# Performance work log

Hardware: AMD Instinct MI355X
Metric: run time of the kernel (lower is better)

## Reference

```python
import jax, jax.numpy as jnp
import numpy as np

BINS = 10

def setup_inputs() -> dict:
    key = jax.random.key(0)
    k1, k2 = jax.random.split(key)
    N, C = 262144, 512
    x = jax.random.normal(k1, (N, C), dtype=jnp.float32)
    target = jax.random.randint(k2, (N,), 0, C, dtype=jnp.int64)
    return {"x": x, "target": target}

def reference(x, target):
    # log-softmax + NLL (reduction='none', no class weights)
    log_p = jax.nn.log_softmax(x, axis=-1)                      # [N, C]
    log_pt = jnp.take_along_axis(log_p, target[:, None].astype(jnp.int32), axis=1)[:, 0]  # [N]
    ce = -log_pt                                                # NLL per-sample
    # gradient-norm proxy g = |pt - 1|, detached
    g = jax.lax.stop_gradient(jnp.abs(jnp.exp(log_pt) - 1.0))   # [N]
    bin_idx = jnp.floor(g * (BINS - 0.0001)).astype(jnp.int32)  # [N] in [0, BINS)
    # histogram (first call: _last_bin_count is None -> raw counts, no EMA)
    bin_count = jnp.zeros((BINS,), dtype=x.dtype).at[bin_idx].add(1.0)
    nonempty = jnp.sum(bin_count > 0).astype(x.dtype)
    gd = jnp.maximum(bin_count * nonempty, 0.0001)
    beta = 1.0 / gd                                             # [BINS]
    loss = jax.lax.stop_gradient(beta[bin_idx]) * ce            # [N]
    return loss.mean()                                          # reduction='mean'
```

## Files before the change

### kernel.cpp

```cpp
#include <hip/hip_runtime.h>
#include <hip/hip_bf16.h>

#define BINS 10
#define C 512

__global__ __launch_bounds__(256) void ghmc_pass1(const float* __restrict__ x,
                                                  const int* __restrict__ target,
                                                  float* __restrict__ gbins,
                                                  int N) {
    __shared__ float s_cnt[BINS];
    __shared__ float s_sum[BINS];
    const int tid = threadIdx.x;
    if (tid < BINS) { s_cnt[tid] = 0.0f; s_sum[tid] = 0.0f; }
    __syncthreads();

    const int sub = tid & 15;
    const int grp = tid >> 4;
    const int row0   = blockIdx.x * 16 + grp;
    const int stride = gridDim.x * 16;

    for (int row = row0; row < N; row += stride) {
        const float* rowp = x + (size_t)row * C;
        const float4* rp4 = (const float4*)rowp;

        float4 v[8];
        #pragma unroll
        for (int j = 0; j < 8; ++j) v[j] = rp4[sub + 16 * j];

        float s = 0.0f;
        #pragma unroll
        for (int j = 0; j < 8; ++j)
            s += __expf(v[j].x) + __expf(v[j].y) + __expf(v[j].z) + __expf(v[j].w);

        #pragma unroll
        for (int off = 8; off >= 1; off >>= 1)
            s += __shfl_xor(s, off);

        float lse = __logf(s);

        int   tgt = target[row];
        float xt  = rowp[tgt];
        float ce  = lse - xt;
        float pt  = __expf(xt - lse);
        float g   = fabsf(pt - 1.0f);
        int   bin = (int)(g * (BINS - 0.0001f));
        bin = bin < 0 ? 0 : (bin > BINS - 1 ? BINS - 1 : bin);

        if (sub == 0) {
            atomicAdd(&s_cnt[bin], 1.0f);
            atomicAdd(&s_sum[bin], ce);
        }
    }

    __syncthreads();
    if (tid < BINS) {
        atomicAdd(&gbins[tid],        s_cnt[tid]);
        atomicAdd(&gbins[BINS + tid], s_sum[tid]);
    }
}

__global__ void ghmc_pass2(const float* __restrict__ gbins,
                           float* __restrict__ out, float invN) {
    if (threadIdx.x == 0 && blockIdx.x == 0) {
        int ne = 0;
        #pragma unroll
        for (int b = 0; b < BINS; ++b)
            if (gbins[b] > 0.0f) ne++;
        float nef = (float)ne;
        float acc = 0.0f;
        #pragma unroll
        for (int b = 0; b < BINS; ++b) {
            float gd = fmaxf(gbins[b] * nef, 0.0001f);
            acc += gbins[BINS + b] / gd;
        }
        out[0] = acc * invN;
    }
}

extern "C" void kernel_launch(void* const* d_in, const int* in_sizes, int n_in,
                              void* d_out, int out_size, void* d_ws, size_t ws_size,
                              hipStream_t stream) {
    const float* x      = (const float*)d_in[0];
    const int*   target = (const int*)d_in[1];
    float*       out    = (float*)d_out;
    float*       gbins  = (float*)d_ws;

    const int N = in_sizes[1];

    hipMemsetAsync(gbins, 0, 2 * BINS * sizeof(float), stream);

    ghmc_pass1<<<2048, 256, 0, stream>>>(x, target, gbins, N);
    ghmc_pass2<<<1, 64, 0, stream>>>(gbins, out, 1.0f / (float)N);
}
```

Measured before the change: 121.9 us.

## Fuse finalize into main kernel via last-block counter and double-row prefetch

Merges the second single-thread finalize kernel into the main kernel using a global atomic ticket counter, so the last block to finish computes the final loss. It also processes two rows per loop iteration, issuing both rows' loads before computing to raise memory-level parallelism. This removes one kernel launch and its gap, at the cost of higher register pressure and a serialized tail in the last block.

```diff
diff --git a/kernel.cpp b/kernel.cpp
--- a/kernel.cpp
+++ b/kernel.cpp
@@ -4,91 +4,123 @@
 #define BINS 10
 #define C 512
 
-__global__ __launch_bounds__(256) void ghmc_pass1(const float* __restrict__ x,
+
+__device__ __forceinline__ void process_row(const float* __restrict__ rowp,
+                                            const float4 (&v)[8],
+                                            int sub, int tgt,
+                                            float* s_cnt, float* s_sum) {
+    float xt = rowp[tgt];
+    float s = 0.0f;
+    #pragma unroll
+    for (int j = 0; j < 8; ++j)
+        s += __expf(v[j].x) + __expf(v[j].y) + __expf(v[j].z) + __expf(v[j].w);
+    #pragma unroll
+    for (int off = 8; off >= 1; off >>= 1)
+        s += __shfl_xor(s, off);
+    float lse = __logf(s);
+    float ce  = lse - xt;
+    float pt  = __expf(xt - lse);
+    float g   = fabsf(pt - 1.0f);
+    int   bin = (int)(g * (BINS - 0.0001f));
+    bin = bin < 0 ? 0 : (bin > BINS - 1 ? BINS - 1 : bin);
+    if (sub == 0) {
+        atomicAdd(&s_cnt[bin], 1.0f);
+        atomicAdd(&s_sum[bin], ce);
+    }
+}
+
+__global__ __launch_bounds__(256) void ghmc_fused(const float* __restrict__ x,
                                                   const int* __restrict__ target,
                                                   float* __restrict__ gbins,
-                                                  int N) {
+                                                  unsigned int* __restrict__ counter,
+                                                  float* __restrict__ out,
+                                                  int N, float invN) {
     __shared__ float s_cnt[BINS];
     __shared__ float s_sum[BINS];
     const int tid = threadIdx.x;
     if (tid < BINS) { s_cnt[tid] = 0.0f; s_sum[tid] = 0.0f; }
     __syncthreads();
 
-    const int sub = tid & 15;
-    const int grp = tid >> 4;
+    const int sub    = tid & 15;
+    const int grp    = tid >> 4;
+    const int stride = gridDim.x * 16;
     const int row0   = blockIdx.x * 16 + grp;
-    const int stride = gridDim.x * 16;
 
-    for (int row = row0; row < N; row += stride) {
-        const float* rowp = x + (size_t)row * C;
-        const float4* rp4 = (const float4*)rowp;
+    for (int row = row0; row < N; row += 2 * stride) {
+        const int rowB = row + stride;
+        const bool hasB = rowB < N;
 
-        float4 v[8];
+        const float* rowpA = x + (size_t)row * C;
+        const float4* rpA  = (const float4*)rowpA;
+        int tgtA = target[row];
+        float4 a[8];
         #pragma unroll
-        for (int j = 0; j < 8; ++j) v[j] = rp4[sub + 16 * j];
+        for (int j = 0; j < 8; ++j) a[j] = rpA[sub + 16 * j];
 
-        float s = 0.0f;
-        #pragma unroll
-        for (int j = 0; j < 8; ++j)
-            s += __expf(v[j].x) + __expf(v[j].y) + __expf(v[j].z) + __expf(v[j].w);
+        const float* rowpB = x + (size_t)rowB * C;
+        const float4* rpB  = (const float4*)rowpB;
+        int tgtB = 0;
+        float4 b[8];
+        if (hasB) {
+            tgtB = target[rowB];
+            #pragma unroll
+            for (int j = 0; j < 8; ++j) b[j] = rpB[sub + 16 * j];
+        }
 
-        #pragma unroll
-        for (int off = 8; off >= 1; off >>= 1)
-            s += __shfl_xor(s, off);
-
-        float lse = __logf(s);
-
-        int   tgt = target[row];
-        float xt  = rowp[tgt];
-        float ce  = lse - xt;
-        float pt  = __expf(xt - lse);
-        float g   = fabsf(pt - 1.0f);
-        int   bin = (int)(g * (BINS - 0.0001f));
-        bin = bin < 0 ? 0 : (bin > BINS - 1 ? BINS - 1 : bin);
-
-        if (sub == 0) {
-            atomicAdd(&s_cnt[bin], 1.0f);
-            atomicAdd(&s_sum[bin], ce);
-        }
+        process_row(rowpA, a, sub, tgtA, s_cnt, s_sum);
+        if (hasB)
+            process_row(rowpB, b, sub, tgtB, s_cnt, s_sum);
     }
 
     __syncthreads();
-    if (tid < BINS) {
-        atomicAdd(&gbins[tid],        s_cnt[tid]);
-        atomicAdd(&gbins[BINS + tid], s_sum[tid]);
-    }
-}
 
-__global__ void ghmc_pass2(const float* __restrict__ gbins,
-                           float* __restrict__ out, float invN) {
-    if (threadIdx.x == 0 && blockIdx.x == 0) {
-        int ne = 0;
+    if (tid == 0) {
+        float keep = 0.0f;
         #pragma unroll
-        for (int b = 0; b < BINS; ++b)
-            if (gbins[b] > 0.0f) ne++;
-        float nef = (float)ne;
-        float acc = 0.0f;
-        #pragma unroll
-        for (int b = 0; b < BINS; ++b) {
-            float gd = fmaxf(gbins[b] * nef, 0.0001f);
-            acc += gbins[BINS + b] / gd;
+        for (int bn = 0; bn < BINS; ++bn) {
+            keep += atomicAdd(&gbins[bn],        s_cnt[bn]);
+            keep += atomicAdd(&gbins[BINS + bn], s_sum[bn]);
         }
-        out[0] = acc * invN;
+        asm volatile("" :: "v"(keep));
+        __threadfence();
+        unsigned int old = atomicAdd(counter, 1u);
+        if (old == gridDim.x - 1) {
+            __threadfence();
+            float cnt[BINS], sm[BINS];
+            #pragma unroll
+            for (int bn = 0; bn < BINS; ++bn) {
+                cnt[bn] = atomicAdd(&gbins[bn], 0.0f);
+                sm[bn]  = atomicAdd(&gbins[BINS + bn], 0.0f);
+            }
+            int ne = 0;
+            #pragma unroll
+            for (int bn = 0; bn < BINS; ++bn)
+                if (cnt[bn] > 0.0f) ne++;
+            float nef = (float)ne;
+            float acc = 0.0f;
+            #pragma unroll
+            for (int bn = 0; bn < BINS; ++bn) {
+                float gd = fmaxf(cnt[bn] * nef, 0.0001f);
+                acc += sm[bn] / gd;
+            }
+            out[0] = acc * invN;
+        }
     }
 }
 
 extern "C" void kernel_launch(void* const* d_in, const int* in_sizes, int n_in,
                               void* d_out, int out_size, void* d_ws, size_t ws_size,
                               hipStream_t stream) {
-    const float* x      = (const float*)d_in[0];
-    const int*   target = (const int*)d_in[1];
-    float*       out    = (float*)d_out;
-    float*       gbins  = (float*)d_ws;
+    const float*  x       = (const float*)d_in[0];
+    const int*    target  = (const int*)d_in[1];
+    float*        out     = (float*)d_out;
+    float*        gbins   = (float*)d_ws;
+    unsigned int* counter = (unsigned int*)((char*)d_ws + 80);
 
     const int N = in_sizes[1];
 
-    hipMemsetAsync(gbins, 0, 2 * BINS * sizeof(float), stream);
+    hipMemsetAsync(d_ws, 0, 96, stream);
 
-    ghmc_pass1<<<2048, 256, 0, stream>>>(x, target, gbins, N);
-    ghmc_pass2<<<1, 64, 0, stream>>>(gbins, out, 1.0f / (float)N);
+    ghmc_fused<<<2048, 256, 0, stream>>>(x, target, gbins, counter, out,
+                                         N, 1.0f / (float)N);
 }
```

Measured after the change: 481.6 us. +295.0%, slower.
